# Performance work log

Hardware: AMD Instinct MI355X
Metric: run time of the kernel (lower is better)

Reference implementation:

```python
import jax, jax.numpy as jnp
import numpy as np

# ---- configuration matching init_kwargs ----
D_IN, D_HID, D_OUT = 4096, 4096, 4096
INTRINSIC = 1024            # size of trainable vector V
BATCH = 512
Q = float(min(np.log(60000.0) ** 2 / INTRINSIC, 1.0))  # fastJL_vars: q = min(ln(60000)^2/d, 1)

PARAM_SHAPES = {
    'W1': (D_HID, D_IN),   # nn.Linear weight is (out, in)
    'b1': (D_HID,),
    'W2': (D_OUT, D_HID),
    'b2': (D_OUT,),
}

def _next_pow2(n):
    return 1 << int(np.ceil(np.log2(n)))

def fwht(x):
    """Fast Walsh-Hadamard transform over a length-2^k vector.
    Mirrors fast_walsh_hadamard_torched: at step i, split axis i of the
    [2]*k view into halves a,b and concatenate (a+b, a-b)."""
    n = x.shape[0]
    steps = int(round(np.log2(n)))
    for i in range(steps):
        y = x.reshape(2 ** i, 2, -1)
        a, b = y[:, 0], y[:, 1]
        x = jnp.stack([a + b, a - b], axis=1).reshape(n)
    return x

def fastjl(V, D, PP, shape):
    """ret = (1/dd) * (PP * FWHT(D * pad(V, LL)))[:DD], reshaped to param shape."""
    LL = D.shape[0]
    dd = V.shape[0]
    DD = int(np.prod(shape))
    v_pad = jnp.zeros((LL,), V.dtype).at[:dd].set(V)
    h = fwht(D * v_pad)
    return ((PP * h)[:DD] / dd).reshape(shape)

def setup_inputs() -> dict:
    key = jax.random.key(0)
    ks = jax.random.split(key, 4 + 3 * len(PARAM_SHAPES) + len(PARAM_SHAPES))
    inp = {}
    inp['x'] = jax.random.normal(ks[0], (BATCH, D_IN), dtype=jnp.float32)
    inp['V'] = jax.random.normal(ks[1], (INTRINSIC,), dtype=jnp.float32) * 0.01
    i = 2
    for name, shape in PARAM_SHAPES.items():
        # initial (frozen) parameter values
        scale = 1.0 / np.sqrt(shape[-1]) if len(shape) > 1 else 0.0
        inp[name + '_init'] = jax.random.normal(ks[i], shape, dtype=jnp.float32) * scale
        LL = _next_pow2(int(np.prod(shape)))
        # D: Rademacher +-1
        rad = jax.random.bernoulli(ks[i + 1], 0.5, (LL,))
        inp['D_' + name] = jnp.where(rad, 1.0, -1.0).astype(jnp.float32)
        # PP = B * R, B ~ Bernoulli(1-q), R ~ N(0, (1/q)^2)
        B = jax.random.bernoulli(ks[i + 2], 1.0 - Q, (LL,)).astype(jnp.float32)
        R = jax.random.normal(ks[i + 3], (LL,), dtype=jnp.float32) * (1.0 / Q)
        inp['PP_' + name] = B * R
        i += 4
    return inp

def reference(x, V, W1_init, b1_init, W2_init, b2_init,
              D_W1, PP_W1, D_b1, PP_b1, D_W2, PP_W2, D_b2, PP_b2):
    # Reconstruct each wrapped-module parameter: init + FastJL(V)
    W1 = W1_init + fastjl(V, D_W1, PP_W1, PARAM_SHAPES['W1'])
    b1 = b1_init + fastjl(V, D_b1, PP_b1, PARAM_SHAPES['b1'])
    W2 = W2_init + fastjl(V, D_W2, PP_W2, PARAM_SHAPES['W2'])
    b2 = b2_init + fastjl(V, D_b2, PP_b2, PARAM_SHAPES['b2'])
    # wrapped module forward: Linear -> ReLU -> Linear
    h = jax.nn.relu(x @ W1.T + b1)
    return h @ W2.T + b2
```

## Files before the change

kernel.cpp:

```cpp
#include <hip/hip_runtime.h>
#include <hip/hip_bf16.h>
#include <stdint.h>

typedef unsigned short u16;
typedef __attribute__((ext_vector_type(8))) short short8;
typedef __attribute__((ext_vector_type(4))) float f32x4;

__device__ __forceinline__ u16 f2bf(float f) {
    union { float f; uint32_t u; } c; c.f = f;
    uint32_t u = c.u;
    u += 0x7fffu + ((u >> 16) & 1u);
    return (u16)(u >> 16);
}

__device__ __forceinline__ void glds16(const void* g, void* l) {
    __builtin_amdgcn_global_load_lds(
        (const __attribute__((address_space(1))) uint32_t*)g,
        (__attribute__((address_space(3))) uint32_t*)l,
        16, 0, 0);
}

__global__ void fwht_g_kernel(const float* __restrict__ V,
                              const float* __restrict__ D0, const float* __restrict__ D1,
                              const float* __restrict__ D2, const float* __restrict__ D3,
                              float* __restrict__ g) {
    __shared__ float s[1024];
    int t = threadIdx.x;
    const float* D = (blockIdx.x == 0) ? D0 : (blockIdx.x == 1) ? D1 :
                     (blockIdx.x == 2) ? D2 : D3;
    s[t] = D[t] * V[t];
    __syncthreads();
    #pragma unroll
    for (int st = 512; st >= 1; st >>= 1) {
        float a = s[t];
        float b = s[t ^ st];
        __syncthreads();
        s[t] = (t & st) ? (b - a) : (a + b);
        __syncthreads();
    }
    g[blockIdx.x * 1024 + t] = s[t] * (1.0f / 1024.0f);
}

__global__ void bias_kernel(const float* __restrict__ init, const float* __restrict__ PP,
                            const float* __restrict__ g, float* __restrict__ out, int n) {
    int i = blockIdx.x * blockDim.x + threadIdx.x;
    if (i < n) out[i] = init[i] + PP[i] * g[i & 1023];
}

__global__ void cast_kernel(const float* __restrict__ in, u16* __restrict__ out, int n4) {
    int i = blockIdx.x * blockDim.x + threadIdx.x;
    if (i >= n4) return;
    float4 v = ((const float4*)in)[i];
    uint32_t lo = (uint32_t)f2bf(v.x) | ((uint32_t)f2bf(v.y) << 16);
    uint32_t hi = (uint32_t)f2bf(v.z) | ((uint32_t)f2bf(v.w) << 16);
    ((uint2*)out)[i] = make_uint2(lo, hi);
}

__global__ void wmat_kernel(const float* __restrict__ init, const float* __restrict__ PP,
                            const float* __restrict__ g, u16* __restrict__ out, int n4) {
    int i = blockIdx.x * blockDim.x + threadIdx.x;
    if (i >= n4) return;
    int e = i * 4;
    float4 wi = ((const float4*)init)[i];
    float4 pp = ((const float4*)PP)[i];
    float4 gv = *((const float4*)(g + (e & 1023)));
    uint32_t lo = (uint32_t)f2bf(wi.x + pp.x * gv.x) | ((uint32_t)f2bf(wi.y + pp.y * gv.y) << 16);
    uint32_t hi = (uint32_t)f2bf(wi.z + pp.z * gv.z) | ((uint32_t)f2bf(wi.w + pp.w * gv.w) << 16);
    ((uint2*)out)[i] = make_uint2(lo, hi);
}

__global__ __launch_bounds__(256) void gemm_splitk(const u16* __restrict__ A,
                                                   const u16* __restrict__ B,
                                                   float* __restrict__ P,
                                                   int M, int N, int K, int Kslice) {
    constexpr int BM = 128, BN = 128, BK = 64;
    __shared__ u16 As[BM * BK];
    __shared__ u16 Bs[BN * BK];

    const int t    = threadIdx.x;
    const int wid  = t >> 6;
    const int lane = t & 63;
    const int wr   = wid >> 1;
    const int wc   = wid & 1;
    const int fr   = lane & 15;
    const int fq   = lane >> 4;

    const int bm = blockIdx.y, bn = blockIdx.x, sk = blockIdx.z;
    const int k_beg = sk * Kslice;
    const u16* Abase = A + (size_t)(bm * BM) * K;
    const u16* Bbase = B + (size_t)(bn * BN) * K;

    f32x4 acc[4][4];
    #pragma unroll
    for (int m = 0; m < 4; ++m)
        #pragma unroll
        for (int n = 0; n < 4; ++n)
            acc[m][n] = (f32x4){0.f, 0.f, 0.f, 0.f};

    for (int k0 = k_beg; k0 < k_beg + Kslice; k0 += BK) {
        #pragma unroll
        for (int q = 0; q < 4; ++q) {
            int L = q * 256 + t;
            int row = L >> 3;
            int cg  = (L & 7) * 8;
            glds16(Abase + (size_t)row * K + k0 + cg, As + L * 8);
        }
        #pragma unroll
        for (int q = 0; q < 4; ++q) {
            int L = q * 256 + t;
            int row = L >> 3;
            int cg  = (L & 7) * 8;
            glds16(Bbase + (size_t)row * K + k0 + cg, Bs + L * 8);
        }
        __syncthreads();

        #pragma unroll
        for (int ks = 0; ks < 2; ++ks) {
            short8 a[4], b[4];
            #pragma unroll
            for (int m = 0; m < 4; ++m)
                a[m] = *(const short8*)(As + (wr * 64 + m * 16 + fr) * BK + ks * 32 + fq * 8);
            #pragma unroll
            for (int n = 0; n < 4; ++n)
                b[n] = *(const short8*)(Bs + (wc * 64 + n * 16 + fr) * BK + ks * 32 + fq * 8);
            #pragma unroll
            for (int m = 0; m < 4; ++m)
                #pragma unroll
                for (int n = 0; n < 4; ++n)
                    acc[m][n] = __builtin_amdgcn_mfma_f32_16x16x32_bf16(a[m], b[n], acc[m][n], 0, 0, 0);
        }
        __syncthreads();
    }

    float* Pp = P + (size_t)sk * M * N;
    #pragma unroll
    for (int m = 0; m < 4; ++m) {
        int grow0 = bm * BM + wr * 64 + m * 16 + fq * 4;
        #pragma unroll
        for (int n = 0; n < 4; ++n) {
            int gcol = bn * BN + wc * 64 + n * 16 + fr;
            #pragma unroll
            for (int j = 0; j < 4; ++j)
                Pp[(size_t)(grow0 + j) * N + gcol] = acc[m][n][j];
        }
    }
}

template <typename OutT, bool RELU, int S>
__global__ void reduce_kernel(const float* __restrict__ P, const float* __restrict__ bias,
                              OutT* __restrict__ out, int MN, int N) {
    int i = blockIdx.x * blockDim.x + threadIdx.x;
    if (i * 4 >= MN) return;
    int e = i * 4;
    int col = e & (N - 1);
    float4 acc = ((const float4*)(P + e))[0];
    #pragma unroll
    for (int s = 1; s < S; ++s) {
        float4 p = ((const float4*)(P + (size_t)s * MN + e))[0];
        acc.x += p.x; acc.y += p.y; acc.z += p.z; acc.w += p.w;
    }
    float4 bv = *((const float4*)(bias + col));
    acc.x += bv.x; acc.y += bv.y; acc.z += bv.z; acc.w += bv.w;
    if (RELU) {
        acc.x = fmaxf(acc.x, 0.f); acc.y = fmaxf(acc.y, 0.f);
        acc.z = fmaxf(acc.z, 0.f); acc.w = fmaxf(acc.w, 0.f);
    }
    if constexpr (sizeof(OutT) == 2) {
        uint32_t lo = (uint32_t)f2bf(acc.x) | ((uint32_t)f2bf(acc.y) << 16);
        uint32_t hi = (uint32_t)f2bf(acc.z) | ((uint32_t)f2bf(acc.w) << 16);
        ((uint2*)out)[i] = make_uint2(lo, hi);
    } else {
        ((float4*)out)[i] = acc;
    }
}

extern "C" void kernel_launch(void* const* d_in, const int* in_sizes, int n_in,
                              void* d_out, int out_size, void* d_ws, size_t ws_size,
                              hipStream_t stream) {
    (void)in_sizes; (void)n_in; (void)out_size; (void)ws_size;

    const float* x       = (const float*)d_in[0];
    const float* V       = (const float*)d_in[1];
    const float* W1_init = (const float*)d_in[2];
    const float* D_W1    = (const float*)d_in[3];
    const float* PP_W1   = (const float*)d_in[4];
    const float* b1_init = (const float*)d_in[5];
    const float* D_b1    = (const float*)d_in[6];
    const float* PP_b1   = (const float*)d_in[7];
    const float* W2_init = (const float*)d_in[8];
    const float* D_W2    = (const float*)d_in[9];
    const float* PP_W2   = (const float*)d_in[10];
    const float* b2_init = (const float*)d_in[11];
    const float* D_b2    = (const float*)d_in[12];
    const float* PP_b2   = (const float*)d_in[13];

    constexpr size_t MB = 1024 * 1024;
    char* ws = (char*)d_ws;
    float* g    = (float*)(ws);
    float* b1w  = (float*)(ws + 16384);
    float* b2w  = (float*)(ws + 32768);
    u16*   xb   = (u16*)(ws + 65536);
    u16*   hb   = (u16*)(ws + 65536 + 4 * MB);
    u16*   wbuf = (u16*)(ws + 65536 + 8 * MB);
    float* Pbuf = (float*)(ws + 65536 + 40 * MB);

    const int M = 512, N = 4096, K = 4096, S = 4, Kslice = K / S;

    fwht_g_kernel<<<4, 1024, 0, stream>>>(V, D_W1, D_b1, D_W2, D_b2, g);
    bias_kernel<<<4, 1024, 0, stream>>>(b1_init, PP_b1, g + 1024, b1w, 4096);
    bias_kernel<<<4, 1024, 0, stream>>>(b2_init, PP_b2, g + 3072, b2w, 4096);
    cast_kernel<<<2048, 256, 0, stream>>>(x, xb, M * K / 4);

    wmat_kernel<<<16384, 256, 0, stream>>>(W1_init, PP_W1, g, wbuf, 4096 * 4096 / 4);
    gemm_splitk<<<dim3(N / 128, M / 128, S), 256, 0, stream>>>(xb, wbuf, Pbuf, M, N, K, Kslice);
    reduce_kernel<u16, true, S><<<M * N / 4 / 256, 256, 0, stream>>>(Pbuf, b1w, hb, M * N, N);

    wmat_kernel<<<16384, 256, 0, stream>>>(W2_init, PP_W2, g + 2048, wbuf, 4096 * 4096 / 4);
    gemm_splitk<<<dim3(N / 128, M / 128, S), 256, 0, stream>>>(hb, wbuf, Pbuf, M, N, K, Kslice);
    reduce_kernel<float, false, S><<<M * N / 4 / 256, 256, 0, stream>>>(Pbuf, b2w, (float*)d_out, M * N, N);
}
```

Baseline: 142.6 us.

## Fuse weight reconstruction into GEMM B-tile load with full-M tiles

Removes the separate wmat kernel that wrote the reconstructed bf16 weight matrix to memory. The GEMM now reads fp32 init and PP directly, applies the FastJL correction and bf16 cast while filling shared memory, and stores the result into the B tile. Tiles are reshaped to cover all 512 rows with 32 columns, so each weight element is read exactly once. The intent is to avoid the bf16 weight write and read-back; the costs are a 64 KB A tile per block, A being reloaded by every column block, and a synchronous B path with no overlap.

After: 150.7 us. 5.7% more time.

```diff
diff --git a/kernel.cpp b/kernel.cpp
--- a/kernel.cpp
+++ b/kernel.cpp
@@ -56,77 +56,68 @@
     ((uint2*)out)[i] = make_uint2(lo, hi);
 }
 
-__global__ void wmat_kernel(const float* __restrict__ init, const float* __restrict__ PP,
-                            const float* __restrict__ g, u16* __restrict__ out, int n4) {
-    int i = blockIdx.x * blockDim.x + threadIdx.x;
-    if (i >= n4) return;
-    int e = i * 4;
-    float4 wi = ((const float4*)init)[i];
-    float4 pp = ((const float4*)PP)[i];
-    float4 gv = *((const float4*)(g + (e & 1023)));
-    uint32_t lo = (uint32_t)f2bf(wi.x + pp.x * gv.x) | ((uint32_t)f2bf(wi.y + pp.y * gv.y) << 16);
-    uint32_t hi = (uint32_t)f2bf(wi.z + pp.z * gv.z) | ((uint32_t)f2bf(wi.w + pp.w * gv.w) << 16);
-    ((uint2*)out)[i] = make_uint2(lo, hi);
-}
-
-__global__ __launch_bounds__(256) void gemm_splitk(const u16* __restrict__ A,
-                                                   const u16* __restrict__ B,
-                                                   float* __restrict__ P,
-                                                   int M, int N, int K, int Kslice) {
-    constexpr int BM = 128, BN = 128, BK = 64;
+__global__ __launch_bounds__(512, 4) void gemm_fused(const u16* __restrict__ A,
+                                                     const float* __restrict__ Winit,
+                                                     const float* __restrict__ PP,
+                                                     const float* __restrict__ gvec,
+                                                     float* __restrict__ P,
+                                                     int M, int N, int K, int Kslice) {
+    constexpr int BM = 512, BN = 32, BK = 64;
     __shared__ u16 As[BM * BK];
     __shared__ u16 Bs[BN * BK];
 
     const int t    = threadIdx.x;
     const int wid  = t >> 6;
     const int lane = t & 63;
-    const int wr   = wid >> 1;
-    const int wc   = wid & 1;
     const int fr   = lane & 15;
     const int fq   = lane >> 4;
 
-    const int bm = blockIdx.y, bn = blockIdx.x, sk = blockIdx.z;
+    const int bn = blockIdx.x, sk = blockIdx.y;
     const int k_beg = sk * Kslice;
-    const u16* Abase = A + (size_t)(bm * BM) * K;
-    const u16* Bbase = B + (size_t)(bn * BN) * K;
-
-    f32x4 acc[4][4];
+
+    const int rowB = t >> 4;
+    const int kkB  = (t & 15) * 4;
+    const float* Wrow = Winit + (size_t)(bn * BN + rowB) * K;
+    const float* Prow = PP    + (size_t)(bn * BN + rowB) * K;
+
+    f32x4 acc[4][2];
     #pragma unroll
     for (int m = 0; m < 4; ++m)
         #pragma unroll
-        for (int n = 0; n < 4; ++n)
+        for (int n = 0; n < 2; ++n)
             acc[m][n] = (f32x4){0.f, 0.f, 0.f, 0.f};
 
     for (int k0 = k_beg; k0 < k_beg + Kslice; k0 += BK) {
         #pragma unroll
-        for (int q = 0; q < 4; ++q) {
-            int L = q * 256 + t;
+        for (int q = 0; q < 8; ++q) {
+            int L = q * 512 + t;
             int row = L >> 3;
             int cg  = (L & 7) * 8;
-            glds16(Abase + (size_t)row * K + k0 + cg, As + L * 8);
-        }
-        #pragma unroll
-        for (int q = 0; q < 4; ++q) {
-            int L = q * 256 + t;
-            int row = L >> 3;
-            int cg  = (L & 7) * 8;
-            glds16(Bbase + (size_t)row * K + k0 + cg, Bs + L * 8);
+            glds16(A + (size_t)row * K + k0 + cg, As + L * 8);
+        }
+        {
+            float4 wi = *(const float4*)(Wrow + k0 + kkB);
+            float4 pp = *(const float4*)(Prow + k0 + kkB);
+            float4 gv = *(const float4*)(gvec + ((k0 + kkB) & 1023));
+            uint32_t lo = (uint32_t)f2bf(wi.x + pp.x * gv.x) | ((uint32_t)f2bf(wi.y + pp.y * gv.y) << 16);
+            uint32_t hi = (uint32_t)f2bf(wi.z + pp.z * gv.z) | ((uint32_t)f2bf(wi.w + pp.w * gv.w) << 16);
+            *(uint2*)(Bs + rowB * BK + kkB) = make_uint2(lo, hi);
         }
         __syncthreads();
 
         #pragma unroll
         for (int ks = 0; ks < 2; ++ks) {
-            short8 a[4], b[4];
+            short8 a[4], b[2];
             #pragma unroll
             for (int m = 0; m < 4; ++m)
-                a[m] = *(const short8*)(As + (wr * 64 + m * 16 + fr) * BK + ks * 32 + fq * 8);
-            #pragma unroll
-            for (int n = 0; n < 4; ++n)
-                b[n] = *(const short8*)(Bs + (wc * 64 + n * 16 + fr) * BK + ks * 32 + fq * 8);
+                a[m] = *(const short8*)(As + (wid * 64 + m * 16 + fr) * BK + ks * 32 + fq * 8);
+            #pragma unroll
+            for (int n = 0; n < 2; ++n)
+                b[n] = *(const short8*)(Bs + (n * 16 + fr) * BK + ks * 32 + fq * 8);
             #pragma unroll
             for (int m = 0; m < 4; ++m)
                 #pragma unroll
-                for (int n = 0; n < 4; ++n)
+                for (int n = 0; n < 2; ++n)
                     acc[m][n] = __builtin_amdgcn_mfma_f32_16x16x32_bf16(a[m], b[n], acc[m][n], 0, 0, 0);
         }
         __syncthreads();
@@ -135,10 +126,10 @@
     float* Pp = P + (size_t)sk * M * N;
     #pragma unroll
     for (int m = 0; m < 4; ++m) {
-        int grow0 = bm * BM + wr * 64 + m * 16 + fq * 4;
-        #pragma unroll
-        for (int n = 0; n < 4; ++n) {
-            int gcol = bn * BN + wc * 64 + n * 16 + fr;
+        int grow0 = wid * 64 + m * 16 + fq * 4;
+        #pragma unroll
+        for (int n = 0; n < 2; ++n) {
+            int gcol = bn * BN + n * 16 + fr;
             #pragma unroll
             for (int j = 0; j < 4; ++j)
                 Pp[(size_t)(grow0 + j) * N + gcol] = acc[m][n][j];
@@ -201,8 +192,7 @@
     float* b2w  = (float*)(ws + 32768);
     u16*   xb   = (u16*)(ws + 65536);
     u16*   hb   = (u16*)(ws + 65536 + 4 * MB);
-    u16*   wbuf = (u16*)(ws + 65536 + 8 * MB);
-    float* Pbuf = (float*)(ws + 65536 + 40 * MB);
+    float* Pbuf = (float*)(ws + 65536 + 8 * MB);
 
     const int M = 512, N = 4096, K = 4096, S = 4, Kslice = K / S;
 
@@ -211,11 +201,9 @@
     bias_kernel<<<4, 1024, 0, stream>>>(b2_init, PP_b2, g + 3072, b2w, 4096);
     cast_kernel<<<2048, 256, 0, stream>>>(x, xb, M * K / 4);
 
-    wmat_kernel<<<16384, 256, 0, stream>>>(W1_init, PP_W1, g, wbuf, 4096 * 4096 / 4);
-    gemm_splitk<<<dim3(N / 128, M / 128, S), 256, 0, stream>>>(xb, wbuf, Pbuf, M, N, K, Kslice);
+    gemm_fused<<<dim3(N / 32, S), 512, 0, stream>>>(xb, W1_init, PP_W1, g, Pbuf, M, N, K, Kslice);
     reduce_kernel<u16, true, S><<<M * N / 4 / 256, 256, 0, stream>>>(Pbuf, b1w, hb, M * N, N);
 
-    wmat_kernel<<<16384, 256, 0, stream>>>(W2_init, PP_W2, g + 2048, wbuf, 4096 * 4096 / 4);
-    gemm_splitk<<<dim3(N / 128, M / 128, S), 256, 0, stream>>>(hb, wbuf, Pbuf, M, N, K, Kslice);
+    gemm_fused<<<dim3(N / 32, S), 512, 0, stream>>>(hb, W2_init, PP_W2, g + 2048, Pbuf, M, N, K, Kslice);
     reduce_kernel<float, false, S><<<M * N / 4 / 256, 256, 0, stream>>>(Pbuf, b2w, (float*)d_out, M * N, N);
 }
```

## Halve GEMM N-tile, XOR-swizzle LDS layout, raise MFMA priority

Applied to the files above, without the earlier changes.

The split-K GEMM tile shrinks from 128x128 to 128x64 and the grid doubles, giving 1024 blocks instead of 512, with launch bounds asking for 4 blocks per CU. LDS tiles are now loaded with an XOR swizzle on the 16-byte column group, and the fragment reads apply the matching XOR, to cut LDS bank conflicts. s_setprio is raised around the MFMA section. The cost is less operand reuse per block, so the A matrix is read from global memory twice as often.

Result: faster. 133.9 us (-6.1%).

```diff
diff --git a/kernel.cpp b/kernel.cpp
--- a/kernel.cpp
+++ b/kernel.cpp
@@ -6,11 +6,11 @@
 typedef __attribute__((ext_vector_type(8))) short short8;
 typedef __attribute__((ext_vector_type(4))) float f32x4;
 
-__device__ __forceinline__ u16 f2bf(float f) {
+__device__ __forceinline__ uint32_t f2bf(float f) {
     union { float f; uint32_t u; } c; c.f = f;
     uint32_t u = c.u;
     u += 0x7fffu + ((u >> 16) & 1u);
-    return (u16)(u >> 16);
+    return u >> 16;
 }
 
 __device__ __forceinline__ void glds16(const void* g, void* l) {
@@ -51,8 +51,8 @@
     int i = blockIdx.x * blockDim.x + threadIdx.x;
     if (i >= n4) return;
     float4 v = ((const float4*)in)[i];
-    uint32_t lo = (uint32_t)f2bf(v.x) | ((uint32_t)f2bf(v.y) << 16);
-    uint32_t hi = (uint32_t)f2bf(v.z) | ((uint32_t)f2bf(v.w) << 16);
+    uint32_t lo = f2bf(v.x) | (f2bf(v.y) << 16);
+    uint32_t hi = f2bf(v.z) | (f2bf(v.w) << 16);
     ((uint2*)out)[i] = make_uint2(lo, hi);
 }
 
@@ -64,16 +64,16 @@
     float4 wi = ((const float4*)init)[i];
     float4 pp = ((const float4*)PP)[i];
     float4 gv = *((const float4*)(g + (e & 1023)));
-    uint32_t lo = (uint32_t)f2bf(wi.x + pp.x * gv.x) | ((uint32_t)f2bf(wi.y + pp.y * gv.y) << 16);
-    uint32_t hi = (uint32_t)f2bf(wi.z + pp.z * gv.z) | ((uint32_t)f2bf(wi.w + pp.w * gv.w) << 16);
+    uint32_t lo = f2bf(wi.x + pp.x * gv.x) | (f2bf(wi.y + pp.y * gv.y) << 16);
+    uint32_t hi = f2bf(wi.z + pp.z * gv.z) | (f2bf(wi.w + pp.w * gv.w) << 16);
     ((uint2*)out)[i] = make_uint2(lo, hi);
 }
 
-__global__ __launch_bounds__(256) void gemm_splitk(const u16* __restrict__ A,
-                                                   const u16* __restrict__ B,
-                                                   float* __restrict__ P,
-                                                   int M, int N, int K, int Kslice) {
-    constexpr int BM = 128, BN = 128, BK = 64;
+__global__ __launch_bounds__(256, 4) void gemm_splitk(const u16* __restrict__ A,
+                                                      const u16* __restrict__ B,
+                                                      float* __restrict__ P,
+                                                      int M, int N, int K, int Kslice) {
+    constexpr int BM = 128, BN = 64, BK = 64;
     __shared__ u16 As[BM * BK];
     __shared__ u16 Bs[BN * BK];
 
@@ -84,51 +84,59 @@
     const int wc   = wid & 1;
     const int fr   = lane & 15;
     const int fq   = lane >> 4;
-
-    const int bm = blockIdx.y, bn = blockIdx.x, sk = blockIdx.z;
+    const int rx   = (fr & 7) << 4;
+
+    const int bn = blockIdx.x, bm = blockIdx.y, sk = blockIdx.z;
     const int k_beg = sk * Kslice;
+
     const u16* Abase = A + (size_t)(bm * BM) * K;
     const u16* Bbase = B + (size_t)(bn * BN) * K;
 
-    f32x4 acc[4][4];
+    f32x4 acc[4][2];
     #pragma unroll
     for (int m = 0; m < 4; ++m)
         #pragma unroll
-        for (int n = 0; n < 4; ++n)
+        for (int n = 0; n < 2; ++n)
             acc[m][n] = (f32x4){0.f, 0.f, 0.f, 0.f};
 
+    #pragma unroll 1
     for (int k0 = k_beg; k0 < k_beg + Kslice; k0 += BK) {
         #pragma unroll
         for (int q = 0; q < 4; ++q) {
             int L = q * 256 + t;
             int row = L >> 3;
-            int cg  = (L & 7) * 8;
-            glds16(Abase + (size_t)row * K + k0 + cg, As + L * 8);
-        }
-        #pragma unroll
-        for (int q = 0; q < 4; ++q) {
+            int cg  = (L & 7) ^ (row & 7);
+            glds16(Abase + (size_t)row * K + k0 + cg * 8, As + L * 8);
+        }
+        #pragma unroll
+        for (int q = 0; q < 2; ++q) {
             int L = q * 256 + t;
             int row = L >> 3;
-            int cg  = (L & 7) * 8;
-            glds16(Bbase + (size_t)row * K + k0 + cg, Bs + L * 8);
-        }
-        __syncthreads();
-
+            int cg  = (L & 7) ^ (row & 7);
+            glds16(Bbase + (size_t)row * K + k0 + cg * 8, Bs + L * 8);
+        }
+        __syncthreads();
+
+        const char* Ap = (const char*)As;
+        const char* Bp = (const char*)Bs;
+        __builtin_amdgcn_s_setprio(1);
         #pragma unroll
         for (int ks = 0; ks < 2; ++ks) {
-            short8 a[4], b[4];
+            const int co = (ks * 64 + fq * 16) ^ rx;
+            short8 a[4], b[2];
             #pragma unroll
             for (int m = 0; m < 4; ++m)
-                a[m] = *(const short8*)(As + (wr * 64 + m * 16 + fr) * BK + ks * 32 + fq * 8);
-            #pragma unroll
-            for (int n = 0; n < 4; ++n)
-                b[n] = *(const short8*)(Bs + (wc * 64 + n * 16 + fr) * BK + ks * 32 + fq * 8);
+                a[m] = *(const short8*)(Ap + (wr * 64 + m * 16 + fr) * 128 + co);
+            #pragma unroll
+            for (int n = 0; n < 2; ++n)
+                b[n] = *(const short8*)(Bp + (wc * 32 + n * 16 + fr) * 128 + co);
             #pragma unroll
             for (int m = 0; m < 4; ++m)
                 #pragma unroll
-                for (int n = 0; n < 4; ++n)
+                for (int n = 0; n < 2; ++n)
                     acc[m][n] = __builtin_amdgcn_mfma_f32_16x16x32_bf16(a[m], b[n], acc[m][n], 0, 0, 0);
         }
+        __builtin_amdgcn_s_setprio(0);
         __syncthreads();
     }
 
@@ -137,8 +145,8 @@
     for (int m = 0; m < 4; ++m) {
         int grow0 = bm * BM + wr * 64 + m * 16 + fq * 4;
         #pragma unroll
-        for (int n = 0; n < 4; ++n) {
-            int gcol = bn * BN + wc * 64 + n * 16 + fr;
+        for (int n = 0; n < 2; ++n) {
+            int gcol = bn * BN + wc * 32 + n * 16 + fr;
             #pragma unroll
             for (int j = 0; j < 4; ++j)
                 Pp[(size_t)(grow0 + j) * N + gcol] = acc[m][n][j];
@@ -166,8 +174,8 @@
         acc.z = fmaxf(acc.z, 0.f); acc.w = fmaxf(acc.w, 0.f);
     }
     if constexpr (sizeof(OutT) == 2) {
-        uint32_t lo = (uint32_t)f2bf(acc.x) | ((uint32_t)f2bf(acc.y) << 16);
-        uint32_t hi = (uint32_t)f2bf(acc.z) | ((uint32_t)f2bf(acc.w) << 16);
+        uint32_t lo = f2bf(acc.x) | (f2bf(acc.y) << 16);
+        uint32_t hi = f2bf(acc.z) | (f2bf(acc.w) << 16);
         ((uint2*)out)[i] = make_uint2(lo, hi);
     } else {
         ((float4*)out)[i] = acc;
@@ -212,10 +220,10 @@
     cast_kernel<<<2048, 256, 0, stream>>>(x, xb, M * K / 4);
 
     wmat_kernel<<<16384, 256, 0, stream>>>(W1_init, PP_W1, g, wbuf, 4096 * 4096 / 4);
-    gemm_splitk<<<dim3(N / 128, M / 128, S), 256, 0, stream>>>(xb, wbuf, Pbuf, M, N, K, Kslice);
+    gemm_splitk<<<dim3(N / 64, M / 128, S), 256, 0, stream>>>(xb, wbuf, Pbuf, M, N, K, Kslice);
     reduce_kernel<u16, true, S><<<M * N / 4 / 256, 256, 0, stream>>>(Pbuf, b1w, hb, M * N, N);
 
     wmat_kernel<<<16384, 256, 0, stream>>>(W2_init, PP_W2, g + 2048, wbuf, 4096 * 4096 / 4);
-    gemm_splitk<<<dim3(N / 128, M / 128, S), 256, 0, stream>>>(hb, wbuf, Pbuf, M, N, K, Kslice);
+    gemm_splitk<<<dim3(N / 64, M / 128, S), 256, 0, stream>>>(hb, wbuf, Pbuf, M, N, K, Kslice);
     reduce_kernel<float, false, S><<<M * N / 4 / 256, 256, 0, stream>>>(Pbuf, b2w, (float*)d_out, M * N, N);
 }
```
